# Performance work log

Measured on AMD Instinct MI355X. Metric: run time of the kernel, lower is better.

The kernel has to match this reference:

```python
import jax, jax.numpy as jnp
import numpy as np

NUM_EXPERTS = 64
TOP_K = 2
NOISE_EPS = 0.01


def setup_inputs() -> dict:
    key = jax.random.key(0)
    k1, k2, k3, k4 = jax.random.split(key, 4)
    B, D, E = 32768, 2048, NUM_EXPERTS
    x = jax.random.normal(k1, (B, D), dtype=jnp.float32)
    # original inits these to zero; use small random weights for a non-degenerate top-k
    w_gate = jax.random.normal(k2, (D, E), dtype=jnp.float32) * 0.02
    w_noise = jax.random.normal(k3, (D, E), dtype=jnp.float32) * 0.02
    noise = jax.random.normal(k4, (B, E), dtype=jnp.float32)  # tf.random.normal draw, fixed
    return {"x": x, "w_gate": w_gate, "w_noise": w_noise, "noise": noise}


def reference(x, w_gate, w_noise, noise):
    # routing_pooling='flatten' on a 2D input is identity
    pooled = x  # [B, D]
    routing = pooled @ w_gate  # [B, E]
    # noisy routing (training=True path)
    noise_stddev = jax.nn.softplus(pooled @ w_noise) + NOISE_EPS
    routing = routing + noise * noise_stddev
    # softmax_top_k: take top k+1, keep top k, softmax, scatter back to E experts
    kk = min(TOP_K + 1, NUM_EXPERTS)
    top_vals, top_idx = jax.lax.top_k(routing, kk)
    top_k_vals = top_vals[:, :TOP_K]            # [B, k]
    top_k_idx = top_idx[:, :TOP_K]              # [B, k]
    top_k_gates = jax.nn.softmax(top_k_vals, axis=-1)
    B = routing.shape[0]
    rows = jnp.arange(B)[:, None]
    # rowwise_unsorted_segment_sum -> scatter gates into expert slots
    out = jnp.zeros((B, NUM_EXPERTS), dtype=routing.dtype).at[rows, top_k_idx].add(top_k_gates)
    return out
```

## Files before the change

kernel.cpp:

```cpp
#include <hip/hip_runtime.h>
#include <math.h>


typedef _Float16 half4v __attribute__((ext_vector_type(4)));
typedef _Float16 half8v __attribute__((ext_vector_type(8)));
typedef float f32x4 __attribute__((ext_vector_type(4)));

constexpr int DIMK = 2048;
constexpr int NEXP = 64;
constexpr int BM   = 64;
constexpr int NCH  = DIMK / 32;

__device__ __forceinline__ void async_load16(const void* g, void* l) {
    __builtin_amdgcn_global_load_lds(
        (const __attribute__((address_space(1))) unsigned int*)g,
        (__attribute__((address_space(3))) unsigned int*)l, 16, 0, 0);
}

__device__ __forceinline__ bool gt_pair(float a, int ia, float b, int ib) {
    return (a > b) || (a == b && ia < ib);
}

__global__ __launch_bounds__(256)
void presplit_kernel(const float* __restrict__ wg, const float* __restrict__ wn,
                     _Float16* __restrict__ wsB)
{
    int gid  = blockIdx.x * 256 + threadIdx.x;
    int lane = gid & 63;
    int t    = (gid >> 6) & 7;
    int c    = gid >> 9;
    int n    = t * 16 + (lane & 15);
    int kb   = c * 32 + ((lane >> 4) << 3);
    const float* src = (n < NEXP) ? (wg + n) : (wn + (n - NEXP));
    half8v h1, h2;
    #pragma unroll
    for (int j = 0; j < 8; ++j) {
        float w = src[(size_t)(kb + j) * NEXP] * 65536.0f;
        _Float16 a = (_Float16)w;
        h1[j] = a;
        h2[j] = (_Float16)(w - (float)a);
    }
    *(half8v*)(wsB + ((((size_t)c * 2 + 0) * 8 + t) * 64 + lane) * 8) = h1;
    *(half8v*)(wsB + ((((size_t)c * 2 + 1) * 8 + t) * 64 + lane) * 8) = h2;
}

__global__ __launch_bounds__(512, 4)
void routing_mfma(const float* __restrict__ x, const _Float16* __restrict__ wsB,
                  const float* __restrict__ noise, float* __restrict__ out)
{
    __shared__ _Float16 Bp[4][2][8][64][8];
    __shared__ float4   cand[BM][2];
    __shared__ float4   res[BM];

    const int tid  = threadIdx.x;
    const int lane = tid & 63;
    const int w    = tid >> 6;
    const int mt   = w >> 1;
    const int wnh  = w & 1;
    const int q    = lane >> 4;
    const int cidx = lane & 15;
    const int row0 = blockIdx.x * BM;

    f32x4  acc[4] = {};
    float4 ra[4][2];
    half8v af0[2], af1[2];

    const float* xr0 = x + (size_t)(row0 + mt * 16 + cidx) * DIMK + q * 8;

    auto issue_B = [&](int c, int buf) {
        #pragma unroll
        for (int ii = 0; ii < 2; ++ii) {
            int idx = w * 2 + ii;
            int p = idx >> 3, t = idx & 7;
            const _Float16* g = wsB + ((((size_t)c * 2 + p) * 8 + t) * 64 + lane) * 8;
            async_load16(g, &Bp[buf][p][t][0][0]);
        }
    };

#define ISSUE_A(C, S)                                            \
    {   const float* pa_ = xr0 + (C) * 32;                       \
        ra[S][0] = *(const float4*)(pa_);                        \
        ra[S][1] = *(const float4*)(pa_ + 4);  }

#define CONVERT(C, P)                                                        \
    {   _Pragma("unroll")                                                    \
        for (int h = 0; h < 2; ++h) {                                        \
            float4 v = ra[(C) & 3][h];                                       \
            float f0 = v.x * 1024.f, f1 = v.y * 1024.f;                      \
            float f2 = v.z * 1024.f, f3 = v.w * 1024.f;                      \
            _Float16 a0 = (_Float16)f0, a1 = (_Float16)f1;                   \
            _Float16 a2 = (_Float16)f2, a3 = (_Float16)f3;                   \
            af0[P][h * 4 + 0] = a0; af0[P][h * 4 + 1] = a1;                  \
            af0[P][h * 4 + 2] = a2; af0[P][h * 4 + 3] = a3;                  \
            af1[P][h * 4 + 0] = (_Float16)(f0 - (float)a0);                  \
            af1[P][h * 4 + 1] = (_Float16)(f1 - (float)a1);                  \
            af1[P][h * 4 + 2] = (_Float16)(f2 - (float)a2);                  \
            af1[P][h * 4 + 3] = (_Float16)(f3 - (float)a3);                  \
        }                                                                    \
    }

#define FENCE() asm volatile("" ::: "memory")

#define STEP(C, ISS, CV, WN)                                                 \
    {                                                                        \
        asm volatile("s_waitcnt vmcnt(" #WN ")" ::: "memory");               \
        asm volatile("s_barrier" ::: "memory");                              \
        if (ISS) issue_B((C) + 3, ((C) + 3) & 3);                            \
        __builtin_amdgcn_s_setprio(1);                                       \
        _Pragma("unroll")                                                    \
        for (int tt = 0; tt < 4; ++tt) {                                     \
            int ntile = (tt < 2) ? (wnh * 2 + tt) : (4 + wnh * 2 + (tt - 2));\
            half8v b0 = *(const half8v*)&Bp[(C) & 3][0][ntile][lane][0];     \
            half8v b1 = *(const half8v*)&Bp[(C) & 3][1][ntile][lane][0];     \
            acc[tt] = __builtin_amdgcn_mfma_f32_16x16x32_f16(                \
                af0[(C) & 1], b0, acc[tt], 0, 0, 0);                         \
            acc[tt] = __builtin_amdgcn_mfma_f32_16x16x32_f16(                \
                af0[(C) & 1], b1, acc[tt], 0, 0, 0);                         \
            acc[tt] = __builtin_amdgcn_mfma_f32_16x16x32_f16(                \
                af1[(C) & 1], b0, acc[tt], 0, 0, 0);                         \
        }                                                                    \
        __builtin_amdgcn_s_setprio(0);                                       \
        if (ISS) ISSUE_A((C) + 3, ((C) + 3) & 3);                            \
        if (CV)  CONVERT((C) + 1, ((C) + 1) & 1);                            \
    }

    issue_B(0, 0);
    ISSUE_A(0, 0);
    FENCE();
    issue_B(1, 1);
    ISSUE_A(1, 1);
    FENCE();
    issue_B(2, 2);
    ISSUE_A(2, 2);
    CONVERT(0, 0);

    #pragma unroll 1
    for (int cb = 0; cb < NCH - 4; cb += 4) {
        STEP(cb + 0, 1, 1, 8)
        STEP(cb + 1, 1, 1, 8)
        STEP(cb + 2, 1, 1, 8)
        STEP(cb + 3, 1, 1, 8)
    }
    STEP(NCH - 4, 1, 1, 8)
    STEP(NCH - 3, 0, 1, 8)
    STEP(NCH - 2, 0, 1, 4)
    STEP(NCH - 1, 0, 0, 0)

#undef STEP
#undef CONVERT
#undef ISSUE_A
#undef FENCE

    const float s = 0x1p-26f;
    {
        float rv[2][4];
        const int rbase = row0 + mt * 16 + q * 4;
        #pragma unroll
        for (int g = 0; g < 2; ++g) {
            int e = wnh * 32 + g * 16 + cidx;
            #pragma unroll
            for (int r = 0; r < 4; ++r) {
                float nz   = noise[(size_t)(rbase + r) * NEXP + e];
                float gate = acc[g][r] * s;
                float nv   = acc[g + 2][r] * s;
                float sp   = fmaxf(nv, 0.f) + log1pf(expf(-fabsf(nv)));
                rv[g][r]   = gate + nz * (sp + 0.01f);
            }
        }
        #pragma unroll
        for (int r = 0; r < 4; ++r) {
            int e0 = wnh * 32 + cidx, e1 = e0 + 16;
            float v1, v2; int i1, i2;
            float a = rv[0][r], b = rv[1][r];
            if (a >= b) { v1 = a; i1 = e0; v2 = b; i2 = e1; }
            else        { v1 = b; i1 = e1; v2 = a; i2 = e0; }
            #pragma unroll
            for (int m = 1; m <= 8; m <<= 1) {
                float b1 = __shfl_xor(v1, m); int ib1 = __shfl_xor(i1, m);
                float b2 = __shfl_xor(v2, m); int ib2 = __shfl_xor(i2, m);
                if (gt_pair(b1, ib1, v1, i1)) {
                    float o1 = v1; int oi1 = i1;
                    v1 = b1; i1 = ib1;
                    if (gt_pair(b2, ib2, o1, oi1)) { v2 = b2; i2 = ib2; }
                    else                           { v2 = o1; i2 = oi1; }
                } else if (gt_pair(b1, ib1, v2, i2)) {
                    v2 = b1; i2 = ib1;
                }
            }
            if (cidx == 0) {
                int rowb = mt * 16 + q * 4 + r;
                cand[rowb][wnh] = make_float4(v1, __int_as_float(i1),
                                              v2, __int_as_float(i2));
            }
        }
    }
    __syncthreads();

    if (tid < BM) {
        float4 c0 = cand[tid][0], c1 = cand[tid][1];
        float mv1 = c0.x; int mi1 = __float_as_int(c0.y);
        float mv2 = c0.z; int mi2 = __float_as_int(c0.w);
        float b1 = c1.x;  int ib1 = __float_as_int(c1.y);
        float b2 = c1.z;  int ib2 = __float_as_int(c1.w);
        if (gt_pair(b1, ib1, mv1, mi1)) {
            float o1 = mv1; int oi1 = mi1;
            mv1 = b1; mi1 = ib1;
            if (gt_pair(b2, ib2, o1, oi1)) { mv2 = b2; mi2 = ib2; }
            else                           { mv2 = o1; mi2 = oi1; }
        } else if (gt_pair(b1, ib1, mv2, mi2)) {
            mv2 = b1; mi2 = ib1;
        }
        float t  = expf(mv2 - mv1);
        float g1 = 1.f / (1.f + t);
        res[tid] = make_float4(g1, __int_as_float(mi1),
                               t * g1, __int_as_float(mi2));
    }
    __syncthreads();

    {
        int rr  = tid >> 3;
        int seg = tid & 7;
        float4 rv = res[rr];
        float g1 = rv.x, g2 = rv.z;
        int   j1 = __float_as_int(rv.y), j2 = __float_as_int(rv.w);
        float* op = out + (size_t)(row0 + rr) * NEXP + seg * 8;
        #pragma unroll
        for (int qq = 0; qq < 2; ++qq) {
            int e0 = seg * 8 + qq * 4;
            float4 o;
            o.x = (e0 + 0 == j1) ? g1 : ((e0 + 0 == j2) ? g2 : 0.f);
            o.y = (e0 + 1 == j1) ? g1 : ((e0 + 1 == j2) ? g2 : 0.f);
            o.z = (e0 + 2 == j1) ? g1 : ((e0 + 2 == j2) ? g2 : 0.f);
            o.w = (e0 + 3 == j1) ? g1 : ((e0 + 3 == j2) ? g2 : 0.f);
            *(float4*)(op + qq * 4) = o;
        }
    }
}

extern "C" void kernel_launch(void* const* d_in, const int* in_sizes, int n_in,
                              void* d_out, int out_size, void* d_ws, size_t ws_size,
                              hipStream_t stream) {
    const float* x     = (const float*)d_in[0];
    const float* wg    = (const float*)d_in[1];
    const float* wn    = (const float*)d_in[2];
    const float* noise = (const float*)d_in[3];
    float* out = (float*)d_out;
    _Float16* wsB = (_Float16*)d_ws;

    presplit_kernel<<<dim3(128), 256, 0, stream>>>(wg, wn, wsB);

    const int Brows = in_sizes[0] / DIMK;
    dim3 grid(Brows / BM);
    routing_mfma<<<grid, 512, 0, stream>>>(x, wsB, noise, out);
}
```

Before: 403.0 us.

## Switch to 32x32x16 MFMA tiles with 256-thread blocks and re-laid-out split weights

```diff
diff --git a/kernel.cpp b/kernel.cpp
--- a/kernel.cpp
+++ b/kernel.cpp
@@ -2,9 +2,9 @@
 #include <math.h>
 
 
-typedef _Float16 half4v __attribute__((ext_vector_type(4)));
 typedef _Float16 half8v __attribute__((ext_vector_type(8)));
-typedef float f32x4 __attribute__((ext_vector_type(4)));
+typedef float f32x4  __attribute__((ext_vector_type(4)));
+typedef float f32x16 __attribute__((ext_vector_type(16)));
 
 constexpr int DIMK = 2048;
 constexpr int NEXP = 64;
@@ -27,157 +27,164 @@
 {
     int gid  = blockIdx.x * 256 + threadIdx.x;
     int lane = gid & 63;
-    int t    = (gid >> 6) & 7;
-    int c    = gid >> 9;
-    int n    = t * 16 + (lane & 15);
-    int kb   = c * 32 + ((lane >> 4) << 3);
-    const float* src = (n < NEXP) ? (wg + n) : (wn + (n - NEXP));
-    half8v h1, h2;
+    int fb   = gid >> 6;
+    int nt   = fb & 3;
+    int p    = (fb >> 2) & 1;
+    int kh   = (fb >> 3) & 1;
+    int c    = fb >> 4;
+    const float* src = (nt < 2) ? (wg + nt * 32 + (lane & 31))
+                                : (wn + (nt - 2) * 32 + (lane & 31));
+    int kb = c * 32 + kh * 16 + ((lane >> 5) << 3);
+    half8v hp;
     #pragma unroll
     for (int j = 0; j < 8; ++j) {
         float w = src[(size_t)(kb + j) * NEXP] * 65536.0f;
         _Float16 a = (_Float16)w;
-        h1[j] = a;
-        h2[j] = (_Float16)(w - (float)a);
-    }
-    *(half8v*)(wsB + ((((size_t)c * 2 + 0) * 8 + t) * 64 + lane) * 8) = h1;
-    *(half8v*)(wsB + ((((size_t)c * 2 + 1) * 8 + t) * 64 + lane) * 8) = h2;
-}
-
-__global__ __launch_bounds__(512, 4)
+        hp[j] = p ? (_Float16)(w - (float)a) : a;
+    }
+    *(half8v*)(wsB + (size_t)fb * 512 + lane * 8) = hp;
+}
+
+__global__ __launch_bounds__(256, 2)
 void routing_mfma(const float* __restrict__ x, const _Float16* __restrict__ wsB,
                   const float* __restrict__ noise, float* __restrict__ out)
 {
-    __shared__ _Float16 Bp[4][2][8][64][8];
+    __shared__ _Float16 Bp[4][16][64][8];
     __shared__ float4   cand[BM][2];
     __shared__ float4   res[BM];
 
     const int tid  = threadIdx.x;
     const int lane = tid & 63;
     const int w    = tid >> 6;
-    const int mt   = w >> 1;
-    const int wnh  = w & 1;
-    const int q    = lane >> 4;
-    const int cidx = lane & 15;
+    const int rg   = w >> 1;
+    const int colh = w & 1;
+    const int m    = lane & 31;
+    const int h    = lane >> 5;
     const int row0 = blockIdx.x * BM;
 
-    f32x4  acc[4] = {};
-    float4 ra[4][2];
-    half8v af0[2], af1[2];
-
-    const float* xr0 = x + (size_t)(row0 + mt * 16 + cidx) * DIMK + q * 8;
+    f32x16 acc[2] = {};
+    float4 ra[4][4];
+    half8v afH[2][2], afL[2][2];
+
+    const float* xp = x + (size_t)(row0 + rg * 32 + m) * DIMK + h * 8;
 
     auto issue_B = [&](int c, int buf) {
         #pragma unroll
-        for (int ii = 0; ii < 2; ++ii) {
-            int idx = w * 2 + ii;
-            int p = idx >> 3, t = idx & 7;
-            const _Float16* g = wsB + ((((size_t)c * 2 + p) * 8 + t) * 64 + lane) * 8;
-            async_load16(g, &Bp[buf][p][t][0][0]);
+        for (int ii = 0; ii < 4; ++ii) {
+            int idx = w * 4 + ii;
+            const _Float16* g = wsB + ((size_t)c * 16 + idx) * 512 + lane * 8;
+            async_load16(g, &Bp[buf][idx][0][0]);
         }
     };
 
-#define ISSUE_A(C, S)                                            \
-    {   const float* pa_ = xr0 + (C) * 32;                       \
-        ra[S][0] = *(const float4*)(pa_);                        \
-        ra[S][1] = *(const float4*)(pa_ + 4);  }
+#define ISSUE_X(C, S)                                            \
+    {   const float* p_ = xp + (C) * 32;                         \
+        ra[S][0] = *(const float4*)(p_);                         \
+        ra[S][1] = *(const float4*)(p_ + 4);                     \
+        ra[S][2] = *(const float4*)(p_ + 16);                    \
+        ra[S][3] = *(const float4*)(p_ + 20);  }
 
 #define CONVERT(C, P)                                                        \
     {   _Pragma("unroll")                                                    \
-        for (int h = 0; h < 2; ++h) {                                        \
-            float4 v = ra[(C) & 3][h];                                       \
-            float f0 = v.x * 1024.f, f1 = v.y * 1024.f;                      \
-            float f2 = v.z * 1024.f, f3 = v.w * 1024.f;                      \
-            _Float16 a0 = (_Float16)f0, a1 = (_Float16)f1;                   \
-            _Float16 a2 = (_Float16)f2, a3 = (_Float16)f3;                   \
-            af0[P][h * 4 + 0] = a0; af0[P][h * 4 + 1] = a1;                  \
-            af0[P][h * 4 + 2] = a2; af0[P][h * 4 + 3] = a3;                  \
-            af1[P][h * 4 + 0] = (_Float16)(f0 - (float)a0);                  \
-            af1[P][h * 4 + 1] = (_Float16)(f1 - (float)a1);                  \
-            af1[P][h * 4 + 2] = (_Float16)(f2 - (float)a2);                  \
-            af1[P][h * 4 + 3] = (_Float16)(f3 - (float)a3);                  \
+        for (int kh = 0; kh < 2; ++kh) {                                     \
+            float4 u = ra[(C) & 3][kh * 2];                                  \
+            float4 v = ra[(C) & 3][kh * 2 + 1];                              \
+            float f0 = u.x * 1024.f, f1 = u.y * 1024.f;                      \
+            float f2 = u.z * 1024.f, f3 = u.w * 1024.f;                      \
+            float f4 = v.x * 1024.f, f5 = v.y * 1024.f;                      \
+            float f6 = v.z * 1024.f, f7 = v.w * 1024.f;                      \
+            _Float16 a0=(_Float16)f0, a1=(_Float16)f1, a2=(_Float16)f2,      \
+                     a3=(_Float16)f3, a4=(_Float16)f4, a5=(_Float16)f5,      \
+                     a6=(_Float16)f6, a7=(_Float16)f7;                       \
+            afH[P][kh][0]=a0; afH[P][kh][1]=a1; afH[P][kh][2]=a2;            \
+            afH[P][kh][3]=a3; afH[P][kh][4]=a4; afH[P][kh][5]=a5;            \
+            afH[P][kh][6]=a6; afH[P][kh][7]=a7;                             \
+            afL[P][kh][0]=(_Float16)(f0-(float)a0);                         \
+            afL[P][kh][1]=(_Float16)(f1-(float)a1);                         \
+            afL[P][kh][2]=(_Float16)(f2-(float)a2);                         \
+            afL[P][kh][3]=(_Float16)(f3-(float)a3);                         \
+            afL[P][kh][4]=(_Float16)(f4-(float)a4);                         \
+            afL[P][kh][5]=(_Float16)(f5-(float)a5);                         \
+            afL[P][kh][6]=(_Float16)(f6-(float)a6);                         \
+            afL[P][kh][7]=(_Float16)(f7-(float)a7);                         \
         }                                                                    \
     }
 
 #define FENCE() asm volatile("" ::: "memory")
 
-#define STEP(C, ISS, CV, WN)                                                 \
+#define STEP(T, ISS, CV, WN)                                                 \
     {                                                                        \
         asm volatile("s_waitcnt vmcnt(" #WN ")" ::: "memory");               \
         asm volatile("s_barrier" ::: "memory");                              \
-        if (ISS) issue_B((C) + 3, ((C) + 3) & 3);                            \
+        if (ISS) { issue_B((T) + 2, ((T) + 2) & 3);                          \
+                   ISSUE_X((T) + 2, ((T) + 2) & 3); }                        \
+        half8v bf[2][2][2];                                                  \
+        _Pragma("unroll")                                                    \
+        for (int kh = 0; kh < 2; ++kh)                                       \
+            _Pragma("unroll")                                                \
+            for (int p = 0; p < 2; ++p)                                      \
+                _Pragma("unroll")                                            \
+                for (int tl = 0; tl < 2; ++tl)                               \
+                    bf[kh][p][tl] = *(const half8v*)                         \
+                        &Bp[(T) & 3][kh * 8 + p * 4 + tl * 2 + colh][lane][0];\
         __builtin_amdgcn_s_setprio(1);                                       \
         _Pragma("unroll")                                                    \
-        for (int tt = 0; tt < 4; ++tt) {                                     \
-            int ntile = (tt < 2) ? (wnh * 2 + tt) : (4 + wnh * 2 + (tt - 2));\
-            half8v b0 = *(const half8v*)&Bp[(C) & 3][0][ntile][lane][0];     \
-            half8v b1 = *(const half8v*)&Bp[(C) & 3][1][ntile][lane][0];     \
-            acc[tt] = __builtin_amdgcn_mfma_f32_16x16x32_f16(                \
-                af0[(C) & 1], b0, acc[tt], 0, 0, 0);                         \
-            acc[tt] = __builtin_amdgcn_mfma_f32_16x16x32_f16(                \
-                af0[(C) & 1], b1, acc[tt], 0, 0, 0);                         \
-            acc[tt] = __builtin_amdgcn_mfma_f32_16x16x32_f16(                \
-                af1[(C) & 1], b0, acc[tt], 0, 0, 0);                         \
-        }                                                                    \
+        for (int tl = 0; tl < 2; ++tl)                                       \
+            _Pragma("unroll")                                                \
+            for (int kh = 0; kh < 2; ++kh) {                                 \
+                acc[tl] = __builtin_amdgcn_mfma_f32_32x32x16_f16(            \
+                    afH[(T) & 1][kh], bf[kh][0][tl], acc[tl], 0, 0, 0);      \
+                acc[tl] = __builtin_amdgcn_mfma_f32_32x32x16_f16(            \
+                    afH[(T) & 1][kh], bf[kh][1][tl], acc[tl], 0, 0, 0);      \
+                acc[tl] = __builtin_amdgcn_mfma_f32_32x32x16_f16(            \
+                    afL[(T) & 1][kh], bf[kh][0][tl], acc[tl], 0, 0, 0);      \
+            }                                                                \
         __builtin_amdgcn_s_setprio(0);                                       \
-        if (ISS) ISSUE_A((C) + 3, ((C) + 3) & 3);                            \
-        if (CV)  CONVERT((C) + 1, ((C) + 1) & 1);                            \
+        if (CV) CONVERT((T) + 1, ((T) + 1) & 1);                             \
     }
 
     issue_B(0, 0);
-    ISSUE_A(0, 0);
+    ISSUE_X(0, 0);
     FENCE();
     issue_B(1, 1);
-    ISSUE_A(1, 1);
-    FENCE();
-    issue_B(2, 2);
-    ISSUE_A(2, 2);
+    ISSUE_X(1, 1);
     CONVERT(0, 0);
 
     #pragma unroll 1
-    for (int cb = 0; cb < NCH - 4; cb += 4) {
-        STEP(cb + 0, 1, 1, 8)
-        STEP(cb + 1, 1, 1, 8)
-        STEP(cb + 2, 1, 1, 8)
-        STEP(cb + 3, 1, 1, 8)
+    for (int t = 0; t < NCH - 4; t += 4) {
+        STEP(t + 0, 1, 1, 8)
+        STEP(t + 1, 1, 1, 8)
+        STEP(t + 2, 1, 1, 8)
+        STEP(t + 3, 1, 1, 8)
     }
     STEP(NCH - 4, 1, 1, 8)
-    STEP(NCH - 3, 0, 1, 8)
-    STEP(NCH - 2, 0, 1, 4)
+    STEP(NCH - 3, 1, 1, 8)
+    STEP(NCH - 2, 0, 1, 8)
     STEP(NCH - 1, 0, 0, 0)
 
 #undef STEP
 #undef CONVERT
-#undef ISSUE_A
+#undef ISSUE_X
 #undef FENCE
 
     const float s = 0x1p-26f;
     {
-        float rv[2][4];
-        const int rbase = row0 + mt * 16 + q * 4;
+        const int e = colh * 32 + m;
         #pragma unroll
-        for (int g = 0; g < 2; ++g) {
-            int e = wnh * 32 + g * 16 + cidx;
+        for (int reg = 0; reg < 16; ++reg) {
+            int r    = (reg & 3) + 8 * (reg >> 2) + 4 * h;
+            int grow = row0 + rg * 32 + r;
+            float nz   = noise[(size_t)grow * NEXP + e];
+            float gate = acc[0][reg] * s;
+            float nv   = acc[1][reg] * s;
+            float sp   = fmaxf(nv, 0.f) + log1pf(expf(-fabsf(nv)));
+            float vv   = gate + nz * (sp + 0.01f);
+            float v1 = vv; int i1 = e;
+            float v2 = -INFINITY; int i2 = 0x7fffffff;
             #pragma unroll
-            for (int r = 0; r < 4; ++r) {
-                float nz   = noise[(size_t)(rbase + r) * NEXP + e];
-                float gate = acc[g][r] * s;
-                float nv   = acc[g + 2][r] * s;
-                float sp   = fmaxf(nv, 0.f) + log1pf(expf(-fabsf(nv)));
-                rv[g][r]   = gate + nz * (sp + 0.01f);
-            }
-        }
-        #pragma unroll
-        for (int r = 0; r < 4; ++r) {
-            int e0 = wnh * 32 + cidx, e1 = e0 + 16;
-            float v1, v2; int i1, i2;
-            float a = rv[0][r], b = rv[1][r];
-            if (a >= b) { v1 = a; i1 = e0; v2 = b; i2 = e1; }
-            else        { v1 = b; i1 = e1; v2 = a; i2 = e0; }
-            #pragma unroll
-            for (int m = 1; m <= 8; m <<= 1) {
-                float b1 = __shfl_xor(v1, m); int ib1 = __shfl_xor(i1, m);
-                float b2 = __shfl_xor(v2, m); int ib2 = __shfl_xor(i2, m);
+            for (int mm = 1; mm <= 16; mm <<= 1) {
+                float b1 = __shfl_xor(v1, mm); int ib1 = __shfl_xor(i1, mm);
+                float b2 = __shfl_xor(v2, mm); int ib2 = __shfl_xor(i2, mm);
                 if (gt_pair(b1, ib1, v1, i1)) {
                     float o1 = v1; int oi1 = i1;
                     v1 = b1; i1 = ib1;
@@ -187,11 +194,9 @@
                     v2 = b1; i2 = ib1;
                 }
             }
-            if (cidx == 0) {
-                int rowb = mt * 16 + q * 4 + r;
-                cand[rowb][wnh] = make_float4(v1, __int_as_float(i1),
-                                              v2, __int_as_float(i2));
-            }
+            if (m == 0)
+                cand[rg * 32 + r][colh] = make_float4(v1, __int_as_float(i1),
+                                                      v2, __int_as_float(i2));
         }
     }
     __syncthreads();
@@ -218,15 +223,15 @@
     __syncthreads();
 
     {
-        int rr  = tid >> 3;
-        int seg = tid & 7;
+        int rr  = tid >> 2;
+        int seg = tid & 3;
         float4 rv = res[rr];
         float g1 = rv.x, g2 = rv.z;
         int   j1 = __float_as_int(rv.y), j2 = __float_as_int(rv.w);
-        float* op = out + (size_t)(row0 + rr) * NEXP + seg * 8;
+        float* op = out + (size_t)(row0 + rr) * NEXP + seg * 16;
         #pragma unroll
-        for (int qq = 0; qq < 2; ++qq) {
-            int e0 = seg * 8 + qq * 4;
+        for (int qq = 0; qq < 4; ++qq) {
+            int e0 = seg * 16 + qq * 4;
             float4 o;
             o.x = (e0 + 0 == j1) ? g1 : ((e0 + 0 == j2) ? g2 : 0.f);
             o.y = (e0 + 1 == j1) ? g1 : ((e0 + 1 == j2) ? g2 : 0.f);
@@ -247,9 +252,9 @@
     float* out = (float*)d_out;
     _Float16* wsB = (_Float16*)d_ws;
 
-    presplit_kernel<<<dim3(128), 256, 0, stream>>>(wg, wn, wsB);
+    presplit_kernel<<<dim3(256), 256, 0, stream>>>(wg, wn, wsB);
 
     const int Brows = in_sizes[0] / DIMK;
     dim3 grid(Brows / BM);
-    routing_mfma<<<grid, 512, 0, stream>>>(x, wsB, noise, out);
-}
+    routing_mfma<<<grid, 256, 0, stream>>>(x, wsB, noise, out);
+}
```

New measurement: 435.8 us. +8.1%, slower.
